# Performance work log

Measured on AMD Instinct MI355X. Metric: run time of the kernel, lower is better.

The kernel has to match this reference:

```python
import jax, jax.numpy as jnp
import numpy as np

B, T, S, H = 8, 256, 256, 512


def setup_inputs() -> dict:
    key = jax.random.key(0)
    k1, k2, k3, k4, k5, k6, k7 = jax.random.split(key, 7)
    query = jax.random.normal(k1, (B, T, H), dtype=jnp.float32)
    encoder_outputs = jax.random.normal(k2, (B, S, H), dtype=jnp.float32)
    src_lengths = jax.random.randint(k3, (B,), 1, S + 1)
    src_lengths = src_lengths.at[0].set(S)  # ensure max(lengths) == S (torch code masks to lengths.max())
    scale = 1.0 / np.sqrt(H)
    W_s = jax.random.normal(k4, (H, H), dtype=jnp.float32) * scale      # nn.Linear(H,H) weight
    W_h = jax.random.normal(k5, (H, H), dtype=jnp.float32) * scale
    v = jax.random.normal(k6, (H,), dtype=jnp.float32) * scale          # nn.Linear(H,1) weight
    W_out = jax.random.normal(k7, (H, 2 * H), dtype=jnp.float32) * scale  # nn.Linear(2H,H) weight
    return {"query": query, "encoder_outputs": encoder_outputs, "src_lengths": src_lengths,
            "W_s": W_s, "W_h": W_h, "v": v, "W_out": W_out}


def reference(query, encoder_outputs, src_lengths, W_s, W_h, v, W_out):
    # torch Linear: y = x @ W.T
    Ws_q = jnp.einsum('bth,oh->bto', query, W_s)            # (B,T,H)
    Wh_e = jnp.einsum('bsh,oh->bso', encoder_outputs, W_h)  # (B,S,H)
    # score(i,j) = v^T tanh(Ws_q_j + Wh_e_i), broadcast over (B,T,S,H)
    energies = jnp.einsum('btsh,h->bts',
                          jnp.tanh(Ws_q[:, :, None, :] + Wh_e[:, None, :, :]), v)
    mask = jnp.arange(encoder_outputs.shape[1]) < src_lengths[:, None]  # (B,S)
    energies = jnp.where(mask[:, None, :], energies, -jnp.inf)
    attn_weights = jax.nn.softmax(energies, axis=-1)        # (B,T,S)
    context = jnp.einsum('bts,bsh->bth', attn_weights, encoder_outputs)
    combined = jnp.concatenate([context, query], axis=-1)   # (B,T,2H)
    attn_out = jnp.tanh(jnp.einsum('btk,ok->bto', combined, W_out))
    return attn_out
```

## Files before the change

kernel.cpp:

```cpp
#include <hip/hip_runtime.h>
#include <hip/hip_bf16.h>


typedef __attribute__((ext_vector_type(8))) short bf16x8;
typedef __attribute__((ext_vector_type(4))) float floatx4;

#define C2LOG2E 2.8853900817779268f
#define LOG2E   1.4426950408889634f
#define NEGBIG  -1e30f

__device__ __forceinline__ float fexp2(float x) { return __builtin_amdgcn_exp2f(x); }
__device__ __forceinline__ float frcp(float x)  { return __builtin_amdgcn_rcpf(x); }
__device__ __forceinline__ float ftanh(float x) {
    return 1.0f - 2.0f * frcp(1.0f + fexp2(C2LOG2E * x));
}
__device__ __forceinline__ float fexp2x(float x) {
    return fexp2(C2LOG2E * x);
}

__device__ __forceinline__ unsigned int f2bf_bits(float f) {
    unsigned int u = __float_as_uint(f);
    return (u + 0x7fffu + ((u >> 16) & 1u)) >> 16;
}

typedef const __attribute__((address_space(1))) unsigned int* gas_u32p;
typedef __attribute__((address_space(3))) unsigned int* las_u32p;
__device__ __forceinline__ void gload16(const void* g, void* l) {
    __builtin_amdgcn_global_load_lds((gas_u32p)g, (las_u32p)l, 16, 0, 0);
}

__global__ __launch_bounds__(256) void cast_all_bf16(
    const float* __restrict__ q,  const float* __restrict__ e,
    const float* __restrict__ Ws, const float* __restrict__ Wh,
    const float* __restrict__ Wo,
    unsigned short* __restrict__ qb,  unsigned short* __restrict__ eb,
    unsigned short* __restrict__ Wsb, unsigned short* __restrict__ Whb,
    unsigned short* __restrict__ Wob)
{
    int blk = blockIdx.x;
    const float* src; unsigned short* dst; int base;
    if      (blk < 1024) { src = q;  dst = qb;  base = blk; }
    else if (blk < 2048) { src = e;  dst = eb;  base = blk - 1024; }
    else if (blk < 2304) { src = Ws; dst = Wsb; base = blk - 2048; }
    else if (blk < 2560) { src = Wh; dst = Whb; base = blk - 2304; }
    else                 { src = Wo; dst = Wob; base = blk - 2560; }
    size_t i = (size_t)base * 1024 + threadIdx.x * 4;
    float4 f = *(const float4*)(src + i);
    ushort4 o;
    o.x = (unsigned short)f2bf_bits(f.x);
    o.y = (unsigned short)f2bf_bits(f.y);
    o.z = (unsigned short)f2bf_bits(f.z);
    o.w = (unsigned short)f2bf_bits(f.w);
    *(ushort4*)(dst + i) = o;
}

__global__ __launch_bounds__(256) void gemm32x64_exp_dual(
    const unsigned short* __restrict__ Xa, const unsigned short* __restrict__ Wa,
    float* __restrict__ Ca,
    const unsigned short* __restrict__ Xb, const unsigned short* __restrict__ Wb_,
    float* __restrict__ Cb)
{
    __shared__ unsigned short sA[32 * 64];
    __shared__ unsigned short sB[64 * 64];
    const int K = 512;
    int blk = blockIdx.x;
    const unsigned short* X; const unsigned short* W; float* C;
    int mt, nt, N;
    if (blk < 512) { X = Xa; W = Wa; C = Ca; N = 512;  mt = blk >> 3; nt = blk & 7; }
    else { blk -= 512; X = Xb; W = Wb_; C = Cb; N = 2048; mt = blk >> 5; nt = blk & 31; }
    int row0 = mt * 32, col0 = nt * 64;
    int tid = threadIdx.x, lane = tid & 63, w = tid >> 6;
    int mw = (w & 1) * 16, nw = (w >> 1) * 32;
    int r = lane & 15;

    int lr  = lane >> 3;
    int csw = ((lane & 7) ^ lr) << 3;
    const unsigned short* gA  = X + (size_t)(row0 + 8 * w + lr) * K + csw;
    const unsigned short* gB0 = W + (size_t)(col0 + 16 * w + lr) * K + csw;
    const unsigned short* gB1 = W + (size_t)(col0 + 16 * w + 8 + lr) * K + csw;
    unsigned short* lA  = &sA[w * 512];
    unsigned short* lB0 = &sB[w * 1024];
    unsigned short* lB1 = &sB[w * 1024 + 512];

    int xr = (r & 7) << 4;
    int cq = (lane >> 4) << 4;
    const char* cA = (const char*)sA;
    const char* cB = (const char*)sB;
    int a0 = (mw + r) * 128 + (cq ^ xr);
    int a1 = (mw + r) * 128 + ((cq + 64) ^ xr);
    int b0 = (nw + r) * 128 + (cq ^ xr);
    int b1 = (nw + r) * 128 + ((cq + 64) ^ xr);

    floatx4 acc0 = {0,0,0,0}, acc1 = {0,0,0,0};
    gload16(gA, lA); gload16(gB0, lB0); gload16(gB1, lB1);

    for (int kb = 0; kb < 8; ++kb) {
        __syncthreads();
        bf16x8 af0 = *(const bf16x8*)(cA + a0);
        bf16x8 af1 = *(const bf16x8*)(cA + a1);
        bf16x8 b00 = *(const bf16x8*)(cB + b0);
        bf16x8 b10 = *(const bf16x8*)(cB + b0 + 2048);
        bf16x8 b01 = *(const bf16x8*)(cB + b1);
        bf16x8 b11 = *(const bf16x8*)(cB + b1 + 2048);
        acc0 = __builtin_amdgcn_mfma_f32_16x16x32_bf16(af0, b00, acc0, 0, 0, 0);
        acc1 = __builtin_amdgcn_mfma_f32_16x16x32_bf16(af0, b10, acc1, 0, 0, 0);
        acc0 = __builtin_amdgcn_mfma_f32_16x16x32_bf16(af1, b01, acc0, 0, 0, 0);
        acc1 = __builtin_amdgcn_mfma_f32_16x16x32_bf16(af1, b11, acc1, 0, 0, 0);
        if (kb < 7) {
            __syncthreads();
            gA += 64; gB0 += 64; gB1 += 64;
            gload16(gA, lA); gload16(gB0, lB0); gload16(gB1, lB1);
        }
    }
    int rq = (lane >> 4) * 4;
    float* cp = C + (size_t)(row0 + mw + rq) * N + col0 + nw + r;
#pragma unroll
    for (int i = 0; i < 4; ++i) {
        cp[(size_t)i * N]      = fexp2x(acc0[i]);
        cp[(size_t)i * N + 16] = fexp2x(acc1[i]);
    }
}

#define TQ 8
__global__ __launch_bounds__(512) void energies_v8(
    const float* __restrict__ EA,
    const float* __restrict__ EBT,
    const float* __restrict__ Vv,
    const int* __restrict__ Len,
    float* __restrict__ E)
{
    __shared__ float sA[TQ][516];
    __shared__ float sWn[512];
    __shared__ float sRed[8][TQ][130];

    int tid  = threadIdx.x;
    int lane = tid & 63;
    int w    = tid >> 6;
    int blk  = blockIdx.x;
    int b    = blk >> 6;
    int j    = (blk >> 5) & 1;
    int tq   = blk & 31;
    int len  = Len[b];
    if (j * 128 >= len) return;
    bool doU1 = (j * 128 + 64) < len;
    int row0g = b * 256 + tq * TQ;

    {
        int t = tid >> 7, c = (tid & 127) * 4;
        *(float4*)&sA[t][c]     = *(const float4*)(EA + (size_t)(row0g + t) * 512 + c);
        *(float4*)&sA[t + 4][c] = *(const float4*)(EA + (size_t)(row0g + t + 4) * 512 + c);
        sWn[tid] = -2.0f * Vv[tid];
    }
    __syncthreads();

    int h0 = w * 64;
    float acc[TQ][2];
#pragma unroll
    for (int t = 0; t < TQ; ++t) { acc[t][0] = 0.f; acc[t][1] = 0.f; }
    const float* bt = EBT + (size_t)h0 * 2048 + b * 256 + j * 128 + lane;

    float B[8] = {0}, P[8] = {0};
#pragma unroll
    for (int i = 0; i < 4; ++i) B[i] = bt[(size_t)i * 2048];
    if (doU1) {
#pragma unroll
        for (int i = 0; i < 4; ++i) B[i + 4] = bt[(size_t)i * 2048 + 64];
    }
#pragma unroll
    for (int hh = 0; hh < 64; hh += 4) {
        if (hh + 4 < 64) {
            const float* nb = bt + (size_t)(hh + 4) * 2048;
#pragma unroll
            for (int i = 0; i < 4; ++i) P[i] = nb[(size_t)i * 2048];
            if (doU1) {
#pragma unroll
                for (int i = 0; i < 4; ++i) P[i + 4] = nb[(size_t)i * 2048 + 64];
            }
        }
        float4 w4 = *(const float4*)&sWn[h0 + hh];
#pragma unroll
        for (int t = 0; t < TQ; ++t) {
            float4 a4 = *(const float4*)&sA[t][h0 + hh];
            {
                float d0 = fmaf(a4.x, B[0], 1.0f);
                float d1 = fmaf(a4.y, B[1], 1.0f);
                float d2 = fmaf(a4.z, B[2], 1.0f);
                float d3 = fmaf(a4.w, B[3], 1.0f);
                float num01 = fmaf(w4.x, d1, w4.y * d0);
                float num23 = fmaf(w4.z, d3, w4.w * d2);
                acc[t][0] = fmaf(num01, frcp(d0 * d1), acc[t][0]);
                acc[t][0] = fmaf(num23, frcp(d2 * d3), acc[t][0]);
            }
            if (doU1) {
                float d0 = fmaf(a4.x, B[4], 1.0f);
                float d1 = fmaf(a4.y, B[5], 1.0f);
                float d2 = fmaf(a4.z, B[6], 1.0f);
                float d3 = fmaf(a4.w, B[7], 1.0f);
                float num01 = fmaf(w4.x, d1, w4.y * d0);
                float num23 = fmaf(w4.z, d3, w4.w * d2);
                acc[t][1] = fmaf(num01, frcp(d0 * d1), acc[t][1]);
                acc[t][1] = fmaf(num23, frcp(d2 * d3), acc[t][1]);
            }
        }
#pragma unroll
        for (int i = 0; i < 8; ++i) B[i] = P[i];
    }

#pragma unroll
    for (int t = 0; t < TQ; ++t) {
        sRed[w][t][lane]      = acc[t][0];
        sRed[w][t][lane + 64] = acc[t][1];
    }
    __syncthreads();
    {
        int s = tid & 127;
#pragma unroll
        for (int half = 0; half < 2; ++half) {
            int t = (tid >> 7) + 4 * half;
            float sum = 0.f;
#pragma unroll
            for (int ww = 0; ww < 8; ++ww) sum += sRed[ww][t][s];
            E[(size_t)(row0g + t) * 256 + j * 128 + s] = sum;
        }
    }
}

__global__ __launch_bounds__(512) void softmax_ctx_fused(
    const float* __restrict__ E,
    const unsigned short* __restrict__ Eb,
    const int* __restrict__ Len,
    unsigned short* __restrict__ Ctx)
{
    __shared__ unsigned short EncT[64][264];
    __shared__ unsigned short sWb[64][264];
    int tid = threadIdx.x, lane = tid & 63, w = tid >> 6;
    int blk = blockIdx.x;
    int b = blk & 7, hq = (blk >> 3) & 7, tg = blk >> 6;
    int len = Len[b];

    {
        int s = tid >> 1, hg = (tid & 1) * 32;
        const ushort4* src = (const ushort4*)(Eb + (size_t)(b * 256 + s) * 512 + hq * 64 + hg);
#pragma unroll
        for (int k = 0; k < 8; ++k) {
            ushort4 u = src[k];
            EncT[hg + k * 4 + 0][s] = u.x;
            EncT[hg + k * 4 + 1][s] = u.y;
            EncT[hg + k * 4 + 2][s] = u.z;
            EncT[hg + k * 4 + 3][s] = u.w;
        }
    }
    for (int i = 0; i < 8; ++i) {
        int row = w * 8 + i;
        const float* erow = E + (size_t)(b * 256 + tg * 64 + row) * 256;
        float ev[4];
#pragma unroll
        for (int j = 0; j < 4; ++j) {
            int s = lane + 64 * j;
            ev[j] = (s < len) ? erow[s] : NEGBIG;
        }
        float m = fmaxf(fmaxf(ev[0], ev[1]), fmaxf(ev[2], ev[3]));
#pragma unroll
        for (int o = 1; o < 64; o <<= 1) m = fmaxf(m, __shfl_xor(m, o, 64));
        float wv[4], wsum = 0.f;
#pragma unroll
        for (int j = 0; j < 4; ++j) { wv[j] = fexp2((ev[j] - m) * LOG2E); wsum += wv[j]; }
#pragma unroll
        for (int o = 1; o < 64; o <<= 1) wsum += __shfl_xor(wsum, o, 64);
        float inv = frcp(wsum);
#pragma unroll
        for (int j = 0; j < 4; ++j)
            sWb[row][lane + 64 * j] = (unsigned short)f2bf_bits(wv[j] * inv);
    }
    __syncthreads();

    int mt = w & 3, npair = w >> 2;
    int t0 = mt * 16;
    int r  = lane & 15, kq = (lane >> 4) * 8;
    int n0 = npair * 32 + r;
    floatx4 acc0 = {0.f,0.f,0.f,0.f}, acc1 = {0.f,0.f,0.f,0.f};
#pragma unroll
    for (int k = 0; k < 8; ++k) {
        bf16x8 a  = *(const bf16x8*)(&sWb[t0 + r][kq + 32 * k]);
        bf16x8 b0 = *(const bf16x8*)(&EncT[n0][kq + 32 * k]);
        bf16x8 b1 = *(const bf16x8*)(&EncT[n0 + 16][kq + 32 * k]);
        acc0 = __builtin_amdgcn_mfma_f32_16x16x32_bf16(a, b0, acc0, 0, 0, 0);
        acc1 = __builtin_amdgcn_mfma_f32_16x16x32_bf16(a, b1, acc1, 0, 0, 0);
    }
    int row0 = (lane >> 4) * 4;
    unsigned short* op = Ctx + (size_t)(b * 256 + tg * 64 + t0 + row0) * 512 + hq * 64 + npair * 32 + r;
#pragma unroll
    for (int i = 0; i < 4; ++i) {
        op[i * 512]      = (unsigned short)f2bf_bits(acc0[i]);
        op[i * 512 + 16] = (unsigned short)f2bf_bits(acc1[i]);
    }
}

__global__ __launch_bounds__(256) void out_gemm32x64_tanh(
    const unsigned short* __restrict__ Ctx, const unsigned short* __restrict__ Q,
    const unsigned short* __restrict__ Wout, float* __restrict__ Out)
{
    __shared__ unsigned short sA[32 * 64];
    __shared__ unsigned short sB[64 * 64];
    const int N = 512, KW = 1024;
    int blk = blockIdx.x;
    int mt = blk >> 3, nt = blk & 7;
    int row0 = mt * 32, col0 = nt * 64;
    int tid = threadIdx.x, lane = tid & 63, w = tid >> 6;
    int mw = (w & 1) * 16, nw = (w >> 1) * 32;
    int r = lane & 15;

    int lr  = lane >> 3;
    int csw = ((lane & 7) ^ lr) << 3;
    const unsigned short* gactx = Ctx  + (size_t)(row0 + 8 * w + lr) * 512 + csw;
    const unsigned short* gaq   = Q    + (size_t)(row0 + 8 * w + lr) * 512 + csw;
    const unsigned short* gB0   = Wout + (size_t)(col0 + 16 * w + lr) * KW + csw;
    const unsigned short* gB1   = Wout + (size_t)(col0 + 16 * w + 8 + lr) * KW + csw;
    unsigned short* lA  = &sA[w * 512];
    unsigned short* lB0 = &sB[w * 1024];
    unsigned short* lB1 = &sB[w * 1024 + 512];

    int xr = (r & 7) << 4;
    int cq = (lane >> 4) << 4;
    const char* cA = (const char*)sA;
    const char* cB = (const char*)sB;
    int a0 = (mw + r) * 128 + (cq ^ xr);
    int a1 = (mw + r) * 128 + ((cq + 64) ^ xr);
    int b0 = (nw + r) * 128 + (cq ^ xr);
    int b1 = (nw + r) * 128 + ((cq + 64) ^ xr);

    floatx4 acc0 = {0,0,0,0}, acc1 = {0,0,0,0};
    gload16(gactx, lA); gload16(gB0, lB0); gload16(gB1, lB1);

    for (int kb = 0; kb < 16; ++kb) {
        __syncthreads();
        bf16x8 af0 = *(const bf16x8*)(cA + a0);
        bf16x8 af1 = *(const bf16x8*)(cA + a1);
        bf16x8 b00 = *(const bf16x8*)(cB + b0);
        bf16x8 b10 = *(const bf16x8*)(cB + b0 + 2048);
        bf16x8 b01 = *(const bf16x8*)(cB + b1);
        bf16x8 b11 = *(const bf16x8*)(cB + b1 + 2048);
        acc0 = __builtin_amdgcn_mfma_f32_16x16x32_bf16(af0, b00, acc0, 0, 0, 0);
        acc1 = __builtin_amdgcn_mfma_f32_16x16x32_bf16(af0, b10, acc1, 0, 0, 0);
        acc0 = __builtin_amdgcn_mfma_f32_16x16x32_bf16(af1, b01, acc0, 0, 0, 0);
        acc1 = __builtin_amdgcn_mfma_f32_16x16x32_bf16(af1, b11, acc1, 0, 0, 0);
        if (kb < 15) {
            __syncthreads();
            int kn = kb + 1;
            const unsigned short* ga = (kn < 8 ? gactx : gaq) + (kn & 7) * 64;
            gB0 += 64; gB1 += 64;
            gload16(ga, lA); gload16(gB0, lB0); gload16(gB1, lB1);
        }
    }
    int rq = (lane >> 4) * 4;
    float* op = Out + (size_t)(row0 + mw + rq) * N + col0 + nw + r;
#pragma unroll
    for (int i = 0; i < 4; ++i) {
        op[(size_t)i * N]      = ftanh(acc0[i]);
        op[(size_t)i * N + 16] = ftanh(acc1[i]);
    }
}

extern "C" void kernel_launch(void* const* d_in, const int* in_sizes, int n_in,
                              void* d_out, int out_size, void* d_ws, size_t ws_size,
                              hipStream_t stream)
{
    const float* query = (const float*)d_in[0];
    const float* enc   = (const float*)d_in[1];
    const int*   len   = (const int*)d_in[2];
    const float* Ws    = (const float*)d_in[3];
    const float* Wh    = (const float*)d_in[4];
    const float* v     = (const float*)d_in[5];
    const float* Wout  = (const float*)d_in[6];
    float* out = (float*)d_out;

    float* EA   = (float*)d_ws;
    float* EBT  = EA + 2048 * 512;
    float* E    = EBT + 512 * 2048;
    unsigned short* qb  = (unsigned short*)(E + 2048 * 256);
    unsigned short* eb  = qb + 2048 * 512;
    unsigned short* Wsb = eb + 2048 * 512;
    unsigned short* Whb = Wsb + 512 * 512;
    unsigned short* Wob = Whb + 512 * 512;
    unsigned short* ctx = Wob + 512 * 1024;

    cast_all_bf16<<<3072, 256, 0, stream>>>(query, enc, Ws, Wh, Wout,
                                            qb, eb, Wsb, Whb, Wob);
    gemm32x64_exp_dual<<<1024, 256, 0, stream>>>(qb, Wsb, EA, Whb, eb, EBT);
    energies_v8<<<512, 512, 0, stream>>>(EA, EBT, v, len, E);
    softmax_ctx_fused<<<256, 512, 0, stream>>>(E, eb, len, ctx);
    out_gemm32x64_tanh<<<512, 256, 0, stream>>>(ctx, qb, Wob, out);
}
```

Measured before the change: 132.4 us.

## Split energies kernel over hidden halves and fewer query rows for more blocks

The energies kernel now splits the hidden dimension into two halves and handles 4 query rows per block instead of 8, raising the grid from 512 to 2048 blocks. Each half writes a separate partial energy buffer, and the softmax kernel adds the two partials when it loads them. The aim is better occupancy and load balance across CUs on the dominant tanh-reduction stage. In exchange, the EBT column loads are amortized over fewer query rows, an extra energy buffer is written and read, and the per-block reduction overhead is paid more often.

Measured after the change: 127.4 us. 3.8% less time.

```diff
diff --git a/kernel.cpp b/kernel.cpp
--- a/kernel.cpp
+++ b/kernel.cpp
@@ -8,6 +8,7 @@
 #define C2LOG2E 2.8853900817779268f
 #define LOG2E   1.4426950408889634f
 #define NEGBIG  -1e30f
+#define TQ 4
 
 __device__ __forceinline__ float fexp2(float x) { return __builtin_amdgcn_exp2f(x); }
 __device__ __forceinline__ float frcp(float x)  { return __builtin_amdgcn_rcpf(x); }
@@ -121,43 +122,43 @@
     }
 }
 
-#define TQ 8
-__global__ __launch_bounds__(512) void energies_v8(
+__global__ __launch_bounds__(512) void energies_v9(
     const float* __restrict__ EA,
     const float* __restrict__ EBT,
     const float* __restrict__ Vv,
     const int* __restrict__ Len,
-    float* __restrict__ E)
-{
-    __shared__ float sA[TQ][516];
-    __shared__ float sWn[512];
+    float* __restrict__ E0,
+    float* __restrict__ E1)
+{
+    __shared__ float sA[TQ][260];
+    __shared__ float sWn[256];
     __shared__ float sRed[8][TQ][130];
 
     int tid  = threadIdx.x;
     int lane = tid & 63;
     int w    = tid >> 6;
     int blk  = blockIdx.x;
-    int b    = blk >> 6;
-    int j    = (blk >> 5) & 1;
-    int tq   = blk & 31;
+    int b    = blk >> 8;
+    int j    = (blk >> 7) & 1;
+    int hf   = (blk >> 6) & 1;
+    int tq   = blk & 63;
     int len  = Len[b];
     if (j * 128 >= len) return;
     bool doU1 = (j * 128 + 64) < len;
     int row0g = b * 256 + tq * TQ;
 
     {
-        int t = tid >> 7, c = (tid & 127) * 4;
-        *(float4*)&sA[t][c]     = *(const float4*)(EA + (size_t)(row0g + t) * 512 + c);
-        *(float4*)&sA[t + 4][c] = *(const float4*)(EA + (size_t)(row0g + t + 4) * 512 + c);
-        sWn[tid] = -2.0f * Vv[tid];
+        int t = tid >> 7, c = (tid & 127) * 2;
+        *(float2*)&sA[t][c] = *(const float2*)(EA + (size_t)(row0g + t) * 512 + hf * 256 + c);
+        if (tid < 256) sWn[tid] = -2.0f * Vv[hf * 256 + tid];
     }
     __syncthreads();
 
-    int h0 = w * 64;
+    int h0 = w * 32;
     float acc[TQ][2];
 #pragma unroll
     for (int t = 0; t < TQ; ++t) { acc[t][0] = 0.f; acc[t][1] = 0.f; }
-    const float* bt = EBT + (size_t)h0 * 2048 + b * 256 + j * 128 + lane;
+    const float* bt = EBT + (size_t)(hf * 256 + h0) * 2048 + b * 256 + j * 128 + lane;
 
     float B[8] = {0}, P[8] = {0};
 #pragma unroll
@@ -167,8 +168,8 @@
         for (int i = 0; i < 4; ++i) B[i + 4] = bt[(size_t)i * 2048 + 64];
     }
 #pragma unroll
-    for (int hh = 0; hh < 64; hh += 4) {
-        if (hh + 4 < 64) {
+    for (int hh = 0; hh < 32; hh += 4) {
+        if (hh + 4 < 32) {
             const float* nb = bt + (size_t)(hh + 4) * 2048;
 #pragma unroll
             for (int i = 0; i < 4; ++i) P[i] = nb[(size_t)i * 2048];
@@ -213,20 +214,18 @@
     }
     __syncthreads();
     {
-        int s = tid & 127;
-#pragma unroll
-        for (int half = 0; half < 2; ++half) {
-            int t = (tid >> 7) + 4 * half;
-            float sum = 0.f;
-#pragma unroll
-            for (int ww = 0; ww < 8; ++ww) sum += sRed[ww][t][s];
-            E[(size_t)(row0g + t) * 256 + j * 128 + s] = sum;
-        }
+        int t = tid >> 7, s = tid & 127;
+        float sum = 0.f;
+#pragma unroll
+        for (int ww = 0; ww < 8; ++ww) sum += sRed[ww][t][s];
+        float* Ep = hf ? E1 : E0;
+        Ep[(size_t)(row0g + t) * 256 + j * 128 + s] = sum;
     }
 }
 
 __global__ __launch_bounds__(512) void softmax_ctx_fused(
-    const float* __restrict__ E,
+    const float* __restrict__ E0,
+    const float* __restrict__ E1,
     const unsigned short* __restrict__ Eb,
     const int* __restrict__ Len,
     unsigned short* __restrict__ Ctx)
@@ -252,12 +251,14 @@
     }
     for (int i = 0; i < 8; ++i) {
         int row = w * 8 + i;
-        const float* erow = E + (size_t)(b * 256 + tg * 64 + row) * 256;
+        size_t ro = (size_t)(b * 256 + tg * 64 + row) * 256;
+        const float* er0 = E0 + ro;
+        const float* er1 = E1 + ro;
         float ev[4];
 #pragma unroll
         for (int j = 0; j < 4; ++j) {
             int s = lane + 64 * j;
-            ev[j] = (s < len) ? erow[s] : NEGBIG;
+            ev[j] = (s < len) ? (er0[s] + er1[s]) : NEGBIG;
         }
         float m = fmaxf(fmaxf(ev[0], ev[1]), fmaxf(ev[2], ev[3]));
 #pragma unroll
@@ -376,8 +377,9 @@
 
     float* EA   = (float*)d_ws;
     float* EBT  = EA + 2048 * 512;
-    float* E    = EBT + 512 * 2048;
-    unsigned short* qb  = (unsigned short*)(E + 2048 * 256);
+    float* E0   = EBT + 512 * 2048;
+    float* E1   = E0 + 2048 * 256;
+    unsigned short* qb  = (unsigned short*)(E1 + 2048 * 256);
     unsigned short* eb  = qb + 2048 * 512;
     unsigned short* Wsb = eb + 2048 * 512;
     unsigned short* Whb = Wsb + 512 * 512;
@@ -387,7 +389,7 @@
     cast_all_bf16<<<3072, 256, 0, stream>>>(query, enc, Ws, Wh, Wout,
                                             qb, eb, Wsb, Whb, Wob);
     gemm32x64_exp_dual<<<1024, 256, 0, stream>>>(qb, Wsb, EA, Whb, eb, EBT);
-    energies_v8<<<512, 512, 0, stream>>>(EA, EBT, v, len, E);
-    softmax_ctx_fused<<<256, 512, 0, stream>>>(E, eb, len, ctx);
+    energies_v9<<<2048, 512, 0, stream>>>(EA, EBT, v, len, E0, E1);
+    softmax_ctx_fused<<<256, 512, 0, stream>>>(E0, E1, eb, len, ctx);
     out_gemm32x64_tanh<<<512, 256, 0, stream>>>(ctx, qb, Wob, out);
 }
```
